# Performance work log

Hardware: AMD Instinct MI355X
Metric: run time of the kernel (lower is better)

Reference implementation:

```python
import jax, jax.numpy as jnp
import numpy as np

N_NODES = 50000


def setup_inputs() -> dict:
    key = jax.random.key(0)
    ks = jax.random.split(key, 10)
    B, N, D, H, O = 2, N_NODES, 128, 128, 10
    x = jax.random.normal(ks[0], (B, N, D), dtype=jnp.float32)
    edge_index = jax.random.randint(ks[1], (2, 800000), 0, N, dtype=jnp.int32)
    s = lambda fan_in: 1.0 / np.sqrt(fan_in)
    W  = jax.random.uniform(ks[2], (D, H), jnp.float32, -s(D), s(D))
    b  = jnp.zeros((H,), jnp.float32)
    W1 = jax.random.uniform(ks[3], (H, H // 2), jnp.float32, -s(H), s(H))
    b1 = jnp.zeros((H // 2,), jnp.float32)
    W2 = jax.random.uniform(ks[4], (H // 2, H // 4), jnp.float32, -s(H // 2), s(H // 2))
    b2 = jnp.zeros((H // 4,), jnp.float32)
    W3 = jax.random.uniform(ks[5], (H // 4, O), jnp.float32, -s(H // 4), s(H // 4))
    b3 = jnp.zeros((O,), jnp.float32)
    return {"x": x, "edge_index": edge_index, "W": W, "b": b,
            "W1": W1, "b1": b1, "W2": W2, "b2": b2, "W3": W3, "b3": b3}


def reference(x, edge_index, W, b, W1, b1, W2, b2, W3, b3):
    # GraphConvolution (Kipf): support = x @ W; out[dst] += support[src]; + b
    src, dst = edge_index[0], edge_index[1]
    support = jnp.einsum("bnd,dh->bnh", x, W)          # [B, N, H]
    msgs = support[:, src, :]                            # [B, E, H] gather
    agg = jnp.zeros_like(support).at[:, dst, :].add(msgs)  # scatter-add
    h = jax.nn.gelu(agg + b, approximate=False)          # GELU (torch default erf)
    # dropout is identity at inference (training=False)
    h = jax.nn.relu(jnp.einsum("bnh,hk->bnk", h, W1) + b1)
    h = jax.nn.relu(jnp.einsum("bnk,km->bnm", h, W2) + b2)
    h = jnp.einsum("bnm,mo->bno", h, W3) + b3            # [B, N, O]
    return h.mean(axis=1)                                # [B, O]
```

## Files before the change

### kernel.cpp

```cpp
#include <hip/hip_runtime.h>
#include <math.h>

#define NN 50000
#define DD 128
#define HH 128
#define L1 64
#define L2 32
#define OO 10

__device__ __forceinline__ float bf2f_lo(unsigned u) { return __uint_as_float(u << 16); }
__device__ __forceinline__ float bf2f_hi(unsigned u) { return __uint_as_float(u & 0xffff0000u); }
__device__ __forceinline__ unsigned short f2bf(float f) {
    unsigned u = __float_as_uint(f);
    return (unsigned short)((u + 0x7fffu + ((u >> 16) & 1u)) >> 16);
}
__device__ __forceinline__ float gelu_f(float v) {
    return 0.5f * v * (1.f + erff(v * 0.70710678118654752f));
}

__global__ __launch_bounds__(256, 4) void k_support(
    const float* __restrict__ x, const float* __restrict__ W,
    unsigned short* __restrict__ supb, int rows,
    const int* __restrict__ ei, int* __restrict__ counts, int E)
{
    __shared__ float xs[64][DD];
    const int tid = threadIdx.x;
    const int row0 = blockIdx.x * 64;

    for (int u = tid * 4; u < 64 * DD; u += 256 * 4) {
        const int r = u >> 7, c = u & 127;
        float4 v = make_float4(0.f, 0.f, 0.f, 0.f);
        if (row0 + r < rows) v = *(const float4*)(x + (size_t)(row0 + r) * DD + c);
        *(float4*)(&xs[r][c]) = v;
    }

    {
        const int chunk = (E + gridDim.x - 1) / gridDim.x;
        const int e0 = blockIdx.x * chunk;
        const int e1 = min(e0 + chunk, E);
        for (int e = e0 + tid; e < e1; e += 256)
            atomicAdd(&counts[ei[(size_t)E + e]], 1);
    }

    const int cg = tid & 31;
    const int rg = tid >> 5;
    float4 acc[8];
    #pragma unroll
    for (int i = 0; i < 8; ++i) acc[i] = make_float4(0.f, 0.f, 0.f, 0.f);
    __syncthreads();

    const float* wp = W + cg * 4;
    #pragma unroll 2
    for (int k = 0; k < DD; k += 4) {
        float4 wv[4];
        #pragma unroll
        for (int jj = 0; jj < 4; ++jj) wv[jj] = *(const float4*)(wp + (size_t)(k + jj) * HH);
        #pragma unroll
        for (int q = 0; q < 2; ++q) {
            #pragma unroll
            for (int i = 0; i < 4; ++i) {
                const float4 xv = *(const float4*)(&xs[q * 32 + rg * 4 + i][k]);
                float4* a = &acc[q * 4 + i];
                a->x = fmaf(xv.x, wv[0].x, fmaf(xv.y, wv[1].x, fmaf(xv.z, wv[2].x, fmaf(xv.w, wv[3].x, a->x))));
                a->y = fmaf(xv.x, wv[0].y, fmaf(xv.y, wv[1].y, fmaf(xv.z, wv[2].y, fmaf(xv.w, wv[3].y, a->y))));
                a->z = fmaf(xv.x, wv[0].z, fmaf(xv.y, wv[1].z, fmaf(xv.z, wv[2].z, fmaf(xv.w, wv[3].z, a->z))));
                a->w = fmaf(xv.x, wv[0].w, fmaf(xv.y, wv[1].w, fmaf(xv.z, wv[2].w, fmaf(xv.w, wv[3].w, a->w))));
            }
        }
    }

    #pragma unroll
    for (int q = 0; q < 2; ++q)
        #pragma unroll
        for (int i = 0; i < 4; ++i) {
            const int r = row0 + q * 32 + rg * 4 + i;
            if (r < rows) {
                const int b = (r >= NN) ? 1 : 0;
                const int n = r - b * NN;
                const size_t sr = (size_t)n * 2 + b;
                const float4 a = acc[q * 4 + i];
                ushort4 o;
                o.x = f2bf(a.x); o.y = f2bf(a.y); o.z = f2bf(a.z); o.w = f2bf(a.w);
                *(ushort4*)(supb + sr * HH + cg * 4) = o;
            }
        }
}

__global__ __launch_bounds__(1024) void k_scan1(
    const int* __restrict__ counts, int* __restrict__ offsets,
    int* __restrict__ blksum, int n)
{
    __shared__ int wsum[16], woff[16];
    const int tid = threadIdx.x, lane = tid & 63, wv = tid >> 6;
    const int i = blockIdx.x * 1024 + tid;
    int v = (i < n) ? counts[i] : 0;
    int x = v;
    #pragma unroll
    for (int d = 1; d < 64; d <<= 1) { int t = __shfl_up(x, d); if (lane >= d) x += t; }
    if (lane == 63) wsum[wv] = x;
    __syncthreads();
    if (wv == 0 && lane < 16) {
        int y = wsum[lane];
        #pragma unroll
        for (int d = 1; d < 16; d <<= 1) { int t = __shfl_up(y, d); if (lane >= d) y += t; }
        woff[lane] = y - wsum[lane];
        if (lane == 15) blksum[blockIdx.x] = y;
    }
    __syncthreads();
    if (i < n) offsets[i] = woff[wv] + (x - v);
}

__global__ __launch_bounds__(1024) void k_scan2(
    int* __restrict__ offsets, const int* __restrict__ blksum, int nblk, int n)
{
    __shared__ int base_sh, tot_sh;
    const int tid = threadIdx.x, lane = tid & 63, wv = tid >> 6;
    if (wv == 0) {
        int v = (lane < nblk) ? blksum[lane] : 0;
        int x = v;
        #pragma unroll
        for (int d = 1; d < 64; d <<= 1) { int t = __shfl_up(x, d); if (lane >= d) x += t; }
        int incl = __shfl(x, blockIdx.x);
        int own  = __shfl(v, blockIdx.x);
        int tot  = __shfl(x, nblk - 1);
        if (lane == 0) { base_sh = incl - own; tot_sh = tot; }
    }
    __syncthreads();
    const int i = blockIdx.x * 1024 + tid;
    if (i < n) offsets[i] += base_sh;
    if (blockIdx.x == nblk - 1 && tid == 0) offsets[n] = tot_sh;
}

__global__ __launch_bounds__(256) void k_bucket(
    const int* __restrict__ ei, const int* __restrict__ offsets,
    int* __restrict__ cursor, int* __restrict__ ss, int E)
{
    int e = blockIdx.x * 256 + threadIdx.x;
    if (e < E) {
        int d = ei[E + e];
        int pos = offsets[d] + atomicAdd(&cursor[d], 1);
        ss[pos] = ei[e];
    }
}

__global__ __launch_bounds__(256) void k_agg(
    const unsigned short* __restrict__ supb, const int* __restrict__ offsets,
    const int* __restrict__ ss, unsigned short* __restrict__ aggb, int nn)
{
    const int tid = threadIdx.x;
    const int lane = tid & 63;
    const int wv = tid >> 6;
    const int d = blockIdx.x * 4 + wv;
    if (d >= nn) return;
    const unsigned short* sp = supb + lane * 4;
    const int s0 = offsets[d], s1 = offsets[d + 1];
    float4 a = make_float4(0.f, 0.f, 0.f, 0.f);
    float4 a2 = make_float4(0.f, 0.f, 0.f, 0.f);
    int i = s0;
    for (; i + 4 <= s1; i += 4) {
        const int sA = ss[i], sB = ss[i + 1], sC = ss[i + 2], sD = ss[i + 3];
        const uint2 rA = *(const uint2*)(sp + (size_t)sA * 256);
        const uint2 rB = *(const uint2*)(sp + (size_t)sB * 256);
        const uint2 rC = *(const uint2*)(sp + (size_t)sC * 256);
        const uint2 rD = *(const uint2*)(sp + (size_t)sD * 256);
        a.x  += bf2f_lo(rA.x); a.y  += bf2f_hi(rA.x); a.z  += bf2f_lo(rA.y); a.w  += bf2f_hi(rA.y);
        a2.x += bf2f_lo(rB.x); a2.y += bf2f_hi(rB.x); a2.z += bf2f_lo(rB.y); a2.w += bf2f_hi(rB.y);
        a.x  += bf2f_lo(rC.x); a.y  += bf2f_hi(rC.x); a.z  += bf2f_lo(rC.y); a.w  += bf2f_hi(rC.y);
        a2.x += bf2f_lo(rD.x); a2.y += bf2f_hi(rD.x); a2.z += bf2f_lo(rD.y); a2.w += bf2f_hi(rD.y);
    }
    for (; i < s1; ++i) {
        const uint2 r = *(const uint2*)(sp + (size_t)ss[i] * 256);
        a.x += bf2f_lo(r.x); a.y += bf2f_hi(r.x); a.z += bf2f_lo(r.y); a.w += bf2f_hi(r.y);
    }
    a.x += a2.x; a.y += a2.y; a.z += a2.z; a.w += a2.w;
    ushort4 o;
    o.x = f2bf(a.x); o.y = f2bf(a.y); o.z = f2bf(a.z); o.w = f2bf(a.w);
    *(ushort4*)(aggb + (size_t)d * 256 + lane * 4) = o;
}

__global__ __launch_bounds__(512) void k_mlp(
    const unsigned short* __restrict__ aggb, const float* __restrict__ b0v,
    const float* __restrict__ W1, const float* __restrict__ b1v,
    const float* __restrict__ W2, const float* __restrict__ b2v,
    float* __restrict__ partials, int srows)
{
    __shared__ float w1s[HH][L1];
    __shared__ float w2s[L1][L2];
    __shared__ float hs[64 * 136];
    __shared__ float b0s[DD], b1s[L1], b2s[L2];
    __shared__ float oacc[64];

    const int tid = threadIdx.x;
    const int row0 = blockIdx.x * 64;

    for (int u = tid * 4; u < HH * L1; u += 2048)
        *(float4*)(&w1s[u >> 6][u & 63]) = *(const float4*)(W1 + u);
    for (int u = tid * 4; u < L1 * L2; u += 2048)
        *(float4*)(&w2s[u >> 5][u & 31]) = *(const float4*)(W2 + u);
    if (tid < DD) b0s[tid] = b0v[tid];
    if (tid < L1) b1s[tid] = b1v[tid];
    if (tid < L2) b2s[tid] = b2v[tid];
    if (tid < 64) oacc[tid] = 0.f;
    __syncthreads();

    for (int u = tid * 8; u < 64 * DD; u += 512 * 8) {
        const int r = u >> 7, c = u & 127;
        float4 g0 = make_float4(0.f, 0.f, 0.f, 0.f);
        float4 g1 = g0;
        if (row0 + r < srows) {
            const uint4 raw = *(const uint4*)(aggb + (size_t)(row0 + r) * HH + c);
            float v[8];
            v[0] = bf2f_lo(raw.x) + b0s[c + 0]; v[1] = bf2f_hi(raw.x) + b0s[c + 1];
            v[2] = bf2f_lo(raw.y) + b0s[c + 2]; v[3] = bf2f_hi(raw.y) + b0s[c + 3];
            v[4] = bf2f_lo(raw.z) + b0s[c + 4]; v[5] = bf2f_hi(raw.z) + b0s[c + 5];
            v[6] = bf2f_lo(raw.w) + b0s[c + 6]; v[7] = bf2f_hi(raw.w) + b0s[c + 7];
            #pragma unroll
            for (int t = 0; t < 8; ++t) v[t] = gelu_f(v[t]);
            g0 = make_float4(v[0], v[1], v[2], v[3]);
            g1 = make_float4(v[4], v[5], v[6], v[7]);
        }
        *(float4*)(&hs[r * 136 + c]) = g0;
        *(float4*)(&hs[r * 136 + c + 4]) = g1;
    }
    __syncthreads();

    const int cg = tid & 15;
    const int rg = tid >> 4;
    float4 acc0 = *(const float4*)(&b1s[cg * 4]);
    float4 acc1 = acc0;
    #pragma unroll 4
    for (int j = 0; j < HH; j += 4) {
        float4 wv[4];
        #pragma unroll
        for (int jj = 0; jj < 4; ++jj) wv[jj] = *(const float4*)(&w1s[j + jj][cg * 4]);
        const float4 h0 = *(const float4*)(&hs[(rg * 2 + 0) * 136 + j]);
        const float4 h1 = *(const float4*)(&hs[(rg * 2 + 1) * 136 + j]);
        acc0.x = fmaf(h0.x, wv[0].x, fmaf(h0.y, wv[1].x, fmaf(h0.z, wv[2].x, fmaf(h0.w, wv[3].x, acc0.x))));
        acc0.y = fmaf(h0.x, wv[0].y, fmaf(h0.y, wv[1].y, fmaf(h0.z, wv[2].y, fmaf(h0.w, wv[3].y, acc0.y))));
        acc0.z = fmaf(h0.x, wv[0].z, fmaf(h0.y, wv[1].z, fmaf(h0.z, wv[2].z, fmaf(h0.w, wv[3].z, acc0.z))));
        acc0.w = fmaf(h0.x, wv[0].w, fmaf(h0.y, wv[1].w, fmaf(h0.z, wv[2].w, fmaf(h0.w, wv[3].w, acc0.w))));
        acc1.x = fmaf(h1.x, wv[0].x, fmaf(h1.y, wv[1].x, fmaf(h1.z, wv[2].x, fmaf(h1.w, wv[3].x, acc1.x))));
        acc1.y = fmaf(h1.x, wv[0].y, fmaf(h1.y, wv[1].y, fmaf(h1.z, wv[2].y, fmaf(h1.w, wv[3].y, acc1.y))));
        acc1.z = fmaf(h1.x, wv[0].z, fmaf(h1.y, wv[1].z, fmaf(h1.z, wv[2].z, fmaf(h1.w, wv[3].z, acc1.z))));
        acc1.w = fmaf(h1.x, wv[0].w, fmaf(h1.y, wv[1].w, fmaf(h1.z, wv[2].w, fmaf(h1.w, wv[3].w, acc1.w))));
    }
    acc0.x = fmaxf(acc0.x, 0.f); acc0.y = fmaxf(acc0.y, 0.f);
    acc0.z = fmaxf(acc0.z, 0.f); acc0.w = fmaxf(acc0.w, 0.f);
    acc1.x = fmaxf(acc1.x, 0.f); acc1.y = fmaxf(acc1.y, 0.f);
    acc1.z = fmaxf(acc1.z, 0.f); acc1.w = fmaxf(acc1.w, 0.f);
    __syncthreads();
    float* h1p = hs;
    *(float4*)(&h1p[(rg * 2 + 0) * 68 + cg * 4]) = acc0;
    *(float4*)(&h1p[(rg * 2 + 1) * 68 + cg * 4]) = acc1;
    __syncthreads();

    float* h2p = hs + 5120;
    {
        const int cg2 = tid & 7;
        const int r2 = tid >> 3;
        float4 a = *(const float4*)(&b2s[cg2 * 4]);
        #pragma unroll 4
        for (int j = 0; j < L1; j += 4) {
            float4 wv[4];
            #pragma unroll
            for (int jj = 0; jj < 4; ++jj) wv[jj] = *(const float4*)(&w2s[j + jj][cg2 * 4]);
            const float4 hv = *(const float4*)(&h1p[r2 * 68 + j]);
            a.x = fmaf(hv.x, wv[0].x, fmaf(hv.y, wv[1].x, fmaf(hv.z, wv[2].x, fmaf(hv.w, wv[3].x, a.x))));
            a.y = fmaf(hv.x, wv[0].y, fmaf(hv.y, wv[1].y, fmaf(hv.z, wv[2].y, fmaf(hv.w, wv[3].y, a.y))));
            a.z = fmaf(hv.x, wv[0].z, fmaf(hv.y, wv[1].z, fmaf(hv.z, wv[2].z, fmaf(hv.w, wv[3].z, a.z))));
            a.w = fmaf(hv.x, wv[0].w, fmaf(hv.y, wv[1].w, fmaf(hv.z, wv[2].w, fmaf(hv.w, wv[3].w, a.w))));
        }
        a.x = fmaxf(a.x, 0.f); a.y = fmaxf(a.y, 0.f);
        a.z = fmaxf(a.z, 0.f); a.w = fmaxf(a.w, 0.f);
        __syncthreads();
        *(float4*)(&h2p[r2 * 36 + cg2 * 4]) = a;
    }
    __syncthreads();

    {
        const int c = tid & 31;
        const int g = tid >> 5;
        float p0 = 0.f, p1 = 0.f;
        #pragma unroll
        for (int i = 0; i < 4; ++i) {
            const int r = g * 4 + i;
            if (row0 + r < srows) {
                const float v = h2p[r * 36 + c];
                if (r & 1) p1 += v; else p0 += v;
            }
        }
        if (p0 != 0.f) atomicAdd(&oacc[c], p0);
        if (p1 != 0.f) atomicAdd(&oacc[32 + c], p1);
    }
    __syncthreads();
    if (tid < 64) partials[(size_t)blockIdx.x * 64 + tid] = oacc[tid];
}

__global__ __launch_bounds__(256) void k_scatter(
    const int* __restrict__ ei, const unsigned short* __restrict__ supb,
    float* __restrict__ aggf, int E)
{
    const int tid = threadIdx.x;
    const int eg = tid >> 6;
    const int lane = tid & 63;
    const int e = blockIdx.x * 4 + eg;
    if (e >= E) return;
    const int src = ei[e];
    const int dst = ei[E + e];
    const uint2 r = *(const uint2*)(supb + (size_t)src * 256 + lane * 4);
    float* ap = aggf + (size_t)dst * 256 + lane * 4;
    unsafeAtomicAdd(ap + 0, bf2f_lo(r.x));
    unsafeAtomicAdd(ap + 1, bf2f_hi(r.x));
    unsafeAtomicAdd(ap + 2, bf2f_lo(r.y));
    unsafeAtomicAdd(ap + 3, bf2f_hi(r.y));
}

__global__ __launch_bounds__(256) void k_cvt(
    const float* __restrict__ in, unsigned short* __restrict__ outb, int n)
{
    int i = blockIdx.x * 256 + threadIdx.x;
    if (i < n) outb[i] = f2bf(in[i]);
}

__global__ __launch_bounds__(256) void k_reduce(
    const float* __restrict__ partials, float* __restrict__ accum, int nblk)
{
    __shared__ float lsum[4][64];
    const int t = threadIdx.x & 63;
    const int w = threadIdx.x >> 6;
    float s = 0.f;
    for (int g = blockIdx.x * 4 + w; g < nblk; g += gridDim.x * 4)
        s += partials[(size_t)g * 64 + t];
    lsum[w][t] = s;
    __syncthreads();
    if (threadIdx.x < 64) {
        const float v = lsum[0][t] + lsum[1][t] + lsum[2][t] + lsum[3][t];
        unsafeAtomicAdd(&accum[t], v);
    }
}

__global__ __launch_bounds__(64) void k_final(
    const float* __restrict__ accum, const float* __restrict__ W3,
    const float* __restrict__ b3v, float* __restrict__ out)
{
    const int tid = threadIdx.x;
    if (tid < 2 * OO) {
        const int b = tid / OO, o = tid % OO;
        float acc = b3v[o];
        const float inv = 1.0f / (float)NN;
        #pragma unroll
        for (int j = 0; j < L2; ++j) acc += (accum[b * 32 + j] * inv) * W3[j * OO + o];
        out[tid] = acc;
    }
}

extern "C" void kernel_launch(void* const* d_in, const int* in_sizes, int n_in,
                              void* d_out, int out_size, void* d_ws, size_t ws_size,
                              hipStream_t stream) {
    const float* x  = (const float*)d_in[0];
    const int*   ei = (const int*)d_in[1];
    const float* W  = (const float*)d_in[2];
    const float* b0 = (const float*)d_in[3];
    const float* W1 = (const float*)d_in[4];
    const float* b1 = (const float*)d_in[5];
    const float* W2 = (const float*)d_in[6];
    const float* b2 = (const float*)d_in[7];
    const float* W3 = (const float*)d_in[8];
    const float* b3 = (const float*)d_in[9];
    float* out = (float*)d_out;

    const int E = in_sizes[1] / 2;
    const int rows = 2 * NN;
    const int nblk = (rows + 63) / 64;
    const int nsb = (NN + 1023) / 1024;

    unsigned short* supb = (unsigned short*)d_ws;
    unsigned short* aggb = supb + (size_t)rows * HH;
    float* partials = (float*)(aggb + (size_t)rows * HH);
    float* accum    = partials + (size_t)nblk * 64;
    int*   counts   = (int*)(accum + 64);
    int*   cursor   = counts + NN;
    int*   offsets  = cursor + NN;
    int*   blksum   = offsets + NN + 1;
    int*   ss       = blksum + 64;
    float* aggf     = (float*)(ss + E);
    const size_t need_csr = ((size_t)rows * HH * 2) * sizeof(unsigned short)
                      + ((size_t)nblk * 64 + 64) * sizeof(float)
                      + ((size_t)NN * 3 + 1 + 64 + E) * sizeof(int);
    const size_t need_fb = need_csr + (size_t)rows * HH * sizeof(float);

    if (ws_size >= need_csr && nsb <= 64) {
        hipMemsetAsync(accum, 0, (64 + 2 * (size_t)NN) * sizeof(int), stream);
        k_support<<<dim3((rows + 63) / 64), dim3(256), 0, stream>>>(x, W, supb, rows, ei, counts, E);
        k_scan1<<<dim3(nsb), dim3(1024), 0, stream>>>(counts, offsets, blksum, NN);
        k_scan2<<<dim3(nsb), dim3(1024), 0, stream>>>(offsets, blksum, nsb, NN);
        k_bucket<<<dim3((E + 255) / 256), dim3(256), 0, stream>>>(ei, offsets, cursor, ss, E);
        k_agg<<<dim3((NN + 3) / 4), dim3(256), 0, stream>>>(supb, offsets, ss, aggb, NN);
        k_mlp<<<dim3(nblk), dim3(512), 0, stream>>>(aggb, b0, W1, b1, W2, b2, partials, rows);
    } else if (ws_size >= need_fb) {
        hipMemsetAsync(accum, 0, 64 * sizeof(float), stream);
        hipMemsetAsync(aggf, 0, (size_t)rows * HH * sizeof(float), stream);
        k_support<<<dim3((rows + 63) / 64), dim3(256), 0, stream>>>(x, W, supb, rows, ei, counts, 0);
        k_scatter<<<dim3((E + 3) / 4), dim3(256), 0, stream>>>(ei, supb, aggf, E);
        k_cvt<<<dim3((rows * HH + 255) / 256), dim3(256), 0, stream>>>(aggf, aggb, rows * HH);
        k_mlp<<<dim3(nblk), dim3(512), 0, stream>>>(aggb, b0, W1, b1, W2, b2, partials, rows);
    }

    k_reduce<<<dim3(64), dim3(256), 0, stream>>>(partials, accum, nblk);
    k_final<<<dim3(1), dim3(64), 0, stream>>>(accum, W3, b3, out);
}
```

Before: 314.8 us.

## Compute support GEMM with bf16 MFMA using pre-transposed padded weights

Replaces the scalar fp32 FMA loop in the support GEMM with bf16 MFMA 16x16x32 instructions. A new prep kernel transposes W into a padded bf16 layout, which each block copies into shared memory. The x tile is converted to bf16 while it is staged. This targets the compute cost of x@W, but adds an extra kernel launch, 52KB of shared memory per block that may reduce occupancy, bf16 rounding of the inputs, and narrower scalar stores of the output.

```diff
diff --git a/kernel.cpp b/kernel.cpp
--- a/kernel.cpp
+++ b/kernel.cpp
@@ -8,6 +8,9 @@
 #define L2 32
 #define OO 10
 
+typedef short v8s __attribute__((ext_vector_type(8)));
+typedef float v4f __attribute__((ext_vector_type(4)));
+
 __device__ __forceinline__ float bf2f_lo(unsigned u) { return __uint_as_float(u << 16); }
 __device__ __forceinline__ float bf2f_hi(unsigned u) { return __uint_as_float(u & 0xffff0000u); }
 __device__ __forceinline__ unsigned short f2bf(float f) {
@@ -18,20 +21,35 @@
     return 0.5f * v * (1.f + erff(v * 0.70710678118654752f));
 }
 
-__global__ __launch_bounds__(256, 4) void k_support(
-    const float* __restrict__ x, const float* __restrict__ W,
+__global__ __launch_bounds__(256) void k_wprep(
+    const float* __restrict__ W, unsigned short* __restrict__ wtb)
+{
+    int i = blockIdx.x * 256 + threadIdx.x;
+    if (i < 128 * 136) {
+        int n = i / 136, k = i % 136;
+        wtb[i] = (k < DD) ? f2bf(W[k * HH + n]) : (unsigned short)0;
+    }
+}
+
+__global__ __launch_bounds__(256) void k_support(
+    const float* __restrict__ x, const unsigned short* __restrict__ wtb,
     unsigned short* __restrict__ supb, int rows,
     const int* __restrict__ ei, int* __restrict__ counts, int E)
 {
-    __shared__ float xs[64][DD];
+    __shared__ __align__(16) unsigned short xs[64 * 136];
+    __shared__ __align__(16) unsigned short wt[128 * 136];
     const int tid = threadIdx.x;
     const int row0 = blockIdx.x * 64;
 
-    for (int u = tid * 4; u < 64 * DD; u += 256 * 4) {
+    for (int u = tid * 4; u < 128 * 136; u += 1024)
+        *(uint2*)(&wt[u]) = *(const uint2*)(wtb + u);
+    for (int u = tid * 4; u < 64 * DD; u += 1024) {
         const int r = u >> 7, c = u & 127;
         float4 v = make_float4(0.f, 0.f, 0.f, 0.f);
         if (row0 + r < rows) v = *(const float4*)(x + (size_t)(row0 + r) * DD + c);
-        *(float4*)(&xs[r][c]) = v;
+        ushort4 o;
+        o.x = f2bf(v.x); o.y = f2bf(v.y); o.z = f2bf(v.z); o.w = f2bf(v.w);
+        *(ushort4*)(&xs[r * 136 + c]) = o;
     }
 
     {
@@ -41,49 +59,42 @@
         for (int e = e0 + tid; e < e1; e += 256)
             atomicAdd(&counts[ei[(size_t)E + e]], 1);
     }
-
-    const int cg = tid & 31;
-    const int rg = tid >> 5;
-    float4 acc[8];
+    __syncthreads();
+
+    const int lane = tid & 63;
+    const int w = tid >> 6;
+    const int m0 = w * 16;
+    const int lm = lane & 15;
+    const int q  = lane >> 4;
+
+    v4f acc[8];
     #pragma unroll
-    for (int i = 0; i < 8; ++i) acc[i] = make_float4(0.f, 0.f, 0.f, 0.f);
-    __syncthreads();
-
-    const float* wp = W + cg * 4;
-    #pragma unroll 2
-    for (int k = 0; k < DD; k += 4) {
-        float4 wv[4];
-        #pragma unroll
-        for (int jj = 0; jj < 4; ++jj) wv[jj] = *(const float4*)(wp + (size_t)(k + jj) * HH);
-        #pragma unroll
-        for (int q = 0; q < 2; ++q) {
-            #pragma unroll
-            for (int i = 0; i < 4; ++i) {
-                const float4 xv = *(const float4*)(&xs[q * 32 + rg * 4 + i][k]);
-                float4* a = &acc[q * 4 + i];
-                a->x = fmaf(xv.x, wv[0].x, fmaf(xv.y, wv[1].x, fmaf(xv.z, wv[2].x, fmaf(xv.w, wv[3].x, a->x))));
-                a->y = fmaf(xv.x, wv[0].y, fmaf(xv.y, wv[1].y, fmaf(xv.z, wv[2].y, fmaf(xv.w, wv[3].y, a->y))));
-                a->z = fmaf(xv.x, wv[0].z, fmaf(xv.y, wv[1].z, fmaf(xv.z, wv[2].z, fmaf(xv.w, wv[3].z, a->z))));
-                a->w = fmaf(xv.x, wv[0].w, fmaf(xv.y, wv[1].w, fmaf(xv.z, wv[2].w, fmaf(xv.w, wv[3].w, a->w))));
+    for (int i = 0; i < 8; ++i) acc[i] = (v4f)(0.f);
+
+    #pragma unroll
+    for (int ks = 0; ks < 4; ++ks) {
+        const int k0 = ks * 32 + q * 8;
+        const v8s af = *(const v8s*)(&xs[(m0 + lm) * 136 + k0]);
+        #pragma unroll
+        for (int ct = 0; ct < 8; ++ct) {
+            const v8s bf = *(const v8s*)(&wt[(ct * 16 + lm) * 136 + k0]);
+            acc[ct] = __builtin_amdgcn_mfma_f32_16x16x32_bf16(af, bf, acc[ct], 0, 0, 0);
+        }
+    }
+
+    #pragma unroll
+    for (int ct = 0; ct < 8; ++ct) {
+        const int col = ct * 16 + lm;
+        #pragma unroll
+        for (int r = 0; r < 4; ++r) {
+            const int rowg = row0 + m0 + q * 4 + r;
+            if (rowg < rows) {
+                const int b = (rowg >= NN) ? 1 : 0;
+                const int n = rowg - b * NN;
+                supb[((size_t)n * 2 + b) * HH + col] = f2bf(acc[ct][r]);
             }
         }
     }
-
-    #pragma unroll
-    for (int q = 0; q < 2; ++q)
-        #pragma unroll
-        for (int i = 0; i < 4; ++i) {
-            const int r = row0 + q * 32 + rg * 4 + i;
-            if (r < rows) {
-                const int b = (r >= NN) ? 1 : 0;
-                const int n = r - b * NN;
-                const size_t sr = (size_t)n * 2 + b;
-                const float4 a = acc[q * 4 + i];
-                ushort4 o;
-                o.x = f2bf(a.x); o.y = f2bf(a.y); o.z = f2bf(a.z); o.w = f2bf(a.w);
-                *(ushort4*)(supb + sr * HH + cg * 4) = o;
-            }
-        }
 }
 
 __global__ __launch_bounds__(1024) void k_scan1(
@@ -382,16 +393,18 @@
     int*   cursor   = counts + NN;
     int*   offsets  = cursor + NN;
     int*   blksum   = offsets + NN + 1;
-    int*   ss       = blksum + 64;
+    unsigned short* wtb = (unsigned short*)(blksum + 64);
+    int*   ss       = (int*)(wtb + 128 * 136);
     float* aggf     = (float*)(ss + E);
-    const size_t need_csr = ((size_t)rows * HH * 2) * sizeof(unsigned short)
+    const size_t need_csr = ((size_t)rows * HH * 2 + 128 * 136) * sizeof(unsigned short)
                       + ((size_t)nblk * 64 + 64) * sizeof(float)
                       + ((size_t)NN * 3 + 1 + 64 + E) * sizeof(int);
     const size_t need_fb = need_csr + (size_t)rows * HH * sizeof(float);
 
     if (ws_size >= need_csr && nsb <= 64) {
         hipMemsetAsync(accum, 0, (64 + 2 * (size_t)NN) * sizeof(int), stream);
-        k_support<<<dim3((rows + 63) / 64), dim3(256), 0, stream>>>(x, W, supb, rows, ei, counts, E);
+        k_wprep<<<dim3((128 * 136 + 255) / 256), dim3(256), 0, stream>>>(W, wtb);
+        k_support<<<dim3((rows + 63) / 64), dim3(256), 0, stream>>>(x, wtb, supb, rows, ei, counts, E);
         k_scan1<<<dim3(nsb), dim3(1024), 0, stream>>>(counts, offsets, blksum, NN);
         k_scan2<<<dim3(nsb), dim3(1024), 0, stream>>>(offsets, blksum, nsb, NN);
         k_bucket<<<dim3((E + 255) / 256), dim3(256), 0, stream>>>(ei, offsets, cursor, ss, E);
@@ -400,7 +413,8 @@
     } else if (ws_size >= need_fb) {
         hipMemsetAsync(accum, 0, 64 * sizeof(float), stream);
         hipMemsetAsync(aggf, 0, (size_t)rows * HH * sizeof(float), stream);
-        k_support<<<dim3((rows + 63) / 64), dim3(256), 0, stream>>>(x, W, supb, rows, ei, counts, 0);
+        k_wprep<<<dim3((128 * 136 + 255) / 256), dim3(256), 0, stream>>>(W, wtb);
+        k_support<<<dim3((rows + 63) / 64), dim3(256), 0, stream>>>(x, wtb, supb, rows, ei, counts, 0);
         k_scatter<<<dim3((E + 3) / 4), dim3(256), 0, stream>>>(ei, supb, aggf, E);
         k_cvt<<<dim3((rows * HH + 255) / 256), dim3(256), 0, stream>>>(aggf, aggb, rows * HH);
         k_mlp<<<dim3(nblk), dim3(512), 0, stream>>>(aggb, b0, W1, b1, W2, b2, partials, rows);
```

New measurement: 310.2 us. About the same (-1.4%).
